# Performance work log

Measured on AMD Instinct MI355X. Metric: run time of the kernel, lower is better.

The kernel has to match this reference:

```python
import jax, jax.numpy as jnp
import numpy as np

H = 2048
NBINS = 256

def setup_inputs() -> dict:
    key = jax.random.key(0)
    k1, k2, k3, k4 = jax.random.split(key, 4)
    input_data = jax.random.uniform(k1, (1, 3, H, H), jnp.float32, -1.0, 1.0)
    target_data = jax.random.uniform(k2, (1, 3, H, H), jnp.float32, -1.0, 1.0)
    mask_src = (jax.random.uniform(k3, (1, 1, H, H)) > 0.5).astype(jnp.float32)
    mask_tar = (jax.random.uniform(k4, (1, 1, H, H)) > 0.5).astype(jnp.float32)
    return {"input_data": input_data, "target_data": target_data,
            "mask_src": mask_src, "mask_tar": mask_tar}


def _de_norm(x):
    # (x+1)/2 clamped to [0,1]
    return jnp.clip((x + 1.0) * 0.5, 0.0, 1.0)


def _masked_cdf(img, mask):
    # img: [3,H,W] in [0,255]; mask: [H,W] 0/1 weights.
    # Equivalent to np.histogram(masked_pixels, bins=256, range=(0,255)) per
    # channel followed by normalized cumsum: weighted bincount over all pixels.
    bins = jnp.clip(jnp.floor(img * (NBINS / 255.0)).astype(jnp.int32), 0, NBINS - 1)
    offs = bins + (jnp.arange(3, dtype=jnp.int32) * NBINS)[:, None, None]
    w = jnp.broadcast_to(mask, img.shape).reshape(-1)
    hist = jax.ops.segment_sum(w, offs.reshape(-1), num_segments=3 * NBINS)
    hist = hist.reshape(3, NBINS)
    cdf = jnp.cumsum(hist, axis=1)
    total = jnp.maximum(cdf[:, -1:], 1.0)  # number of masked pixels
    return cdf / total


def _cal_trans(dst_cdf, ref_cdf):
    # Faithful vectorization of PSGAN cal_trans: for i in 1..255, table[i] is
    # the first j in 1..255 with ref_cdf[j-1] <= dst_cdf[i] <= ref_cdf[j],
    # else i; table[0]=0, table[255]=255.
    j0 = jnp.searchsorted(ref_cdf, dst_cdf, side='left')
    cand = jnp.clip(j0, 1, NBINS - 1)
    ok = (ref_cdf[cand - 1] <= dst_cdf) & (ref_cdf[cand] >= dst_cdf)
    idx = jnp.arange(NBINS)
    table = jnp.where(ok, cand, idx)
    table = table.at[0].set(0).at[NBINS - 1].set(NBINS - 1)
    return table


def _histogram_loss(input_data, target_data, mask_src, mask_tar):
    inp = _de_norm(input_data)[0] * 255.0   # [3,H,W]
    tar = _de_norm(target_data)[0] * 255.0  # [3,H,W]
    ms = mask_src[0, 0]  # [H,W]
    mt = mask_tar[0, 0]
    input_masked = inp * ms
    target_masked = tar * mt

    cdf_dst = _masked_cdf(input_masked, ms)   # [3,256]
    cdf_ref = _masked_cdf(target_masked, mt)  # [3,256]
    tables = jax.vmap(_cal_trans)(cdf_dst, cdf_ref)  # [3,256] int

    # remap masked pixels through per-channel LUT (int() truncation)
    pix = jnp.clip(input_masked.astype(jnp.int32), 0, NBINS - 1)  # [3,H,W]
    matched = jnp.take_along_axis(tables, pix.reshape(3, -1), axis=1)
    matched = matched.reshape(input_masked.shape).astype(input_masked.dtype)
    input_match = jnp.where(ms[None] != 0, matched, input_masked)
    input_match = jax.lax.stop_gradient(input_match)  # to_var(requires_grad=False)

    return jnp.mean(jnp.abs(input_masked - input_match))


def reference(input_data, target_data, mask_src, mask_tar):
    return _histogram_loss(input_data, target_data, mask_src, mask_tar)
```

## Files before the change

### kernel.cpp

```cpp
#include <hip/hip_runtime.h>

#define HH 2048
#define NPIX (HH * HH)
#define NBINS 256
#define NRBINS 512
#define NQ (NPIX / 4)

#define BLOCKS 512
#define THREADS 512
#define ITERS (NQ / (BLOCKS * THREADS))

#define CNT_SHIFT 42
#define FRAC_MASK ((1ULL << CNT_SHIFT) - 1)

#define GPK_WORDS (3 * NRBINS)
#define GHT_WORDS (3 * NBINS)
#define WS_ZERO_BYTES (GPK_WORDS * 8 + GHT_WORDS * 4)

__device__ __forceinline__ float denorm255(float x) {
    return fminf(fmaxf((x + 1.0f) * 0.5f, 0.0f), 1.0f) * 255.0f;
}

__global__ __launch_bounds__(THREADS, 2) void fused_hist(
        const float* __restrict__ in, const float* __restrict__ tar,
        const float* __restrict__ ms, const float* __restrict__ mt,
        unsigned long long* __restrict__ gpk, unsigned* __restrict__ ght) {
    __shared__ unsigned long long lpk[3 * NRBINS];
    __shared__ unsigned lht[3 * NBINS];
    for (int i = threadIdx.x; i < 3 * NRBINS; i += THREADS) lpk[i] = 0ULL;
    for (int i = threadIdx.x; i < 3 * NBINS; i += THREADS) lht[i] = 0u;
    __syncthreads();

    const float BSCALE = 256.0f / 255.0f;
    const float FSCALE = 4194304.0f;
    const int stride = BLOCKS * THREADS;
    int idx = blockIdx.x * THREADS + threadIdx.x;

    float4 cm  = ((const float4*)ms)[idx];
    float4 ct  = ((const float4*)mt)[idx];
    float4 ca0 = ((const float4*)(in))[idx];
    float4 ca1 = ((const float4*)(in + NPIX))[idx];
    float4 ca2 = ((const float4*)(in + 2 * NPIX))[idx];
    float4 cb0 = ((const float4*)(tar))[idx];
    float4 cb1 = ((const float4*)(tar + NPIX))[idx];
    float4 cb2 = ((const float4*)(tar + 2 * NPIX))[idx];

    #pragma unroll
    for (int s = 0; s < ITERS; ++s) {
        float4 nm, nt4, na0, na1, na2, nb0, nb1, nb2;
        const int nidx = idx + stride;
        if (s < ITERS - 1) {
            nm  = ((const float4*)ms)[nidx];
            nt4 = ((const float4*)mt)[nidx];
            na0 = ((const float4*)(in))[nidx];
            na1 = ((const float4*)(in + NPIX))[nidx];
            na2 = ((const float4*)(in + 2 * NPIX))[nidx];
            nb0 = ((const float4*)(tar))[nidx];
            nb1 = ((const float4*)(tar + NPIX))[nidx];
            nb2 = ((const float4*)(tar + 2 * NPIX))[nidx];
        }

        const float mv[4] = {cm.x, cm.y, cm.z, cm.w};
        const float tv[4] = {ct.x, ct.y, ct.z, ct.w};
        const float av[3][4] = {{ca0.x, ca0.y, ca0.z, ca0.w},
                                {ca1.x, ca1.y, ca1.z, ca1.w},
                                {ca2.x, ca2.y, ca2.z, ca2.w}};
        const float bv[3][4] = {{cb0.x, cb0.y, cb0.z, cb0.w},
                                {cb1.x, cb1.y, cb1.z, cb1.w},
                                {cb2.x, cb2.y, cb2.z, cb2.w}};

        #pragma unroll
        for (int ch = 0; ch < 3; ++ch) {
            #pragma unroll
            for (int k = 0; k < 4; ++k) {
                float v = denorm255(av[ch][k]);
                int hb = min((int)(v * BSCALE), NBINS - 1);
                int tb = (int)v;
                unsigned fr = (unsigned)((v - (float)tb) * FSCALE);
                unsigned long long pk =
                    (1ULL << CNT_SHIFT) | (unsigned long long)fr;
                pk = (mv[k] != 0.0f) ? pk : 0ULL;
                atomicAdd(&lpk[ch * NRBINS + hb + tb], pk);

                float w = denorm255(bv[ch][k]);
                int wb = min((int)(w * BSCALE), NBINS - 1);
                atomicAdd(&lht[ch * NBINS + wb], (tv[k] != 0.0f) ? 1u : 0u);
            }
        }
        if (s < ITERS - 1) {
            cm = nm; ct = nt4;
            ca0 = na0; ca1 = na1; ca2 = na2;
            cb0 = nb0; cb1 = nb1; cb2 = nb2;
        }
        idx = nidx;
    }
    __syncthreads();
    for (int i = threadIdx.x; i < 3 * NRBINS; i += THREADS) {
        unsigned long long p = lpk[i];
        if (p) atomicAdd(&gpk[i], p);
    }
    for (int i = threadIdx.x; i < 3 * NBINS; i += THREADS) {
        unsigned h = lht[i];
        if (h) atomicAdd(&ght[i], h);
    }
}

__global__ __launch_bounds__(NBINS) void table_loss(
        const unsigned long long* __restrict__ gpk,
        const unsigned* __restrict__ ght, float* __restrict__ out) {
    __shared__ float cdf[6][NBINS];
    __shared__ float tot[6];
    const int t = threadIdx.x;

    unsigned long long pe[3], po[3];
    #pragma unroll
    for (int ch = 0; ch < 3; ++ch) {
        pe[ch] = gpk[ch * NRBINS + 2 * t];
        po[ch] = gpk[ch * NRBINS + 2 * t + 1];
        unsigned long long pp = (t > 0) ? gpk[ch * NRBINS + 2 * t - 1] : 0ULL;
        cdf[ch][t] = (float)((pe[ch] >> CNT_SHIFT) + (pp >> CNT_SHIFT));
        cdf[3 + ch][t] = (float)ght[ch * NBINS + t];
    }
    __syncthreads();
    #pragma unroll
    for (int off = 1; off < NBINS; off <<= 1) {
        float add[6];
        #pragma unroll
        for (int j = 0; j < 6; ++j) add[j] = (t >= off) ? cdf[j][t - off] : 0.0f;
        __syncthreads();
        #pragma unroll
        for (int j = 0; j < 6; ++j) cdf[j][t] += add[j];
        __syncthreads();
    }
    if (t < 6) tot[t] = fmaxf(cdf[t][NBINS - 1], 1.0f);
    __syncthreads();
    #pragma unroll
    for (int j = 0; j < 6; ++j) cdf[j][t] = cdf[j][t] / tot[j];
    __syncthreads();

    double lsum = 0.0;
    #pragma unroll
    for (int ch = 0; ch < 3; ++ch) {
        const float d = cdf[ch][t];
        const float* ref = cdf[3 + ch];
        int lo = 0, hi = NBINS;
        while (lo < hi) {
            int mid = (lo + hi) >> 1;
            if (ref[mid] < d) lo = mid + 1; else hi = mid;
        }
        int cand = min(max(lo, 1), NBINS - 1);
        int T = (ref[cand - 1] <= d && ref[cand] >= d) ? cand : t;
        if (t == 0) T = 0;
        if (t == NBINS - 1) T = NBINS - 1;

        const int b = t;
        const double c =
            (double)((pe[ch] >> CNT_SHIFT) + (po[ch] >> CNT_SHIFT));
        const double F =
            (double)((pe[ch] & FRAC_MASK) + (po[ch] & FRAC_MASK)) *
            (1.0 / 4194304.0);
        lsum += (T <= b) ? (c * (double)(b - T) + F)
                         : (c * (double)(T - b) - F);
    }
    #pragma unroll
    for (int off = 32; off; off >>= 1) lsum += __shfl_down(lsum, off, 64);
    __shared__ double wsum[4];
    if ((t & 63) == 0) wsum[t >> 6] = lsum;
    __syncthreads();
    if (t == 0)
        out[0] = (float)((wsum[0] + wsum[1] + wsum[2] + wsum[3]) /
                         (double)(3 * NPIX));
}

extern "C" void kernel_launch(void* const* d_in, const int* in_sizes, int n_in,
                              void* d_out, int out_size, void* d_ws, size_t ws_size,
                              hipStream_t stream) {
    const float* in  = (const float*)d_in[0];
    const float* tar = (const float*)d_in[1];
    const float* ms  = (const float*)d_in[2];
    const float* mt  = (const float*)d_in[3];
    float* out = (float*)d_out;

    unsigned long long* gpk = (unsigned long long*)d_ws;
    unsigned* ght = (unsigned*)((char*)d_ws + GPK_WORDS * 8);

    hipMemsetAsync(d_ws, 0, WS_ZERO_BYTES, stream);
    fused_hist<<<BLOCKS, THREADS, 0, stream>>>(in, tar, ms, mt, gpk, ght);
    table_loss<<<1, NBINS, 0, stream>>>(gpk, ght, out);
}
```

Baseline: 160.7 us.

## Split source and target histograms into separate block roles with mask-predicated atomics

The fused histogram kernel now launches twice as many blocks, half building the source packed histogram and half the target histogram, each reading only its own four input planes. Explicit register prefetching is removed in favour of more resident blocks (launch bounds raised to 8 per CU) and less shared memory per block. Atomics are skipped for unmasked pixels instead of adding zero, which roughly halves the number of LDS atomics on this input. The cost is more global merge atomics from twice the blocks and divergent branches inside wavefronts.

```diff
diff --git a/kernel.cpp b/kernel.cpp
--- a/kernel.cpp
+++ b/kernel.cpp
@@ -6,9 +6,14 @@
 #define NRBINS 512
 #define NQ (NPIX / 4)
 
-#define BLOCKS 512
 #define THREADS 512
-#define ITERS (NQ / (BLOCKS * THREADS))
+#define SRC_BLOCKS 1024
+#define TAR_BLOCKS 1024
+#define GRID (SRC_BLOCKS + TAR_BLOCKS)
+#define SRC_CHUNK (NQ / SRC_BLOCKS)
+#define TAR_CHUNK (NQ / TAR_BLOCKS)
+#define SRC_ITERS (SRC_CHUNK / THREADS)
+#define TAR_ITERS (TAR_CHUNK / THREADS)
 
 #define CNT_SHIFT 42
 #define FRAC_MASK ((1ULL << CNT_SHIFT) - 1)
@@ -21,87 +26,82 @@
     return fminf(fmaxf((x + 1.0f) * 0.5f, 0.0f), 1.0f) * 255.0f;
 }
 
-__global__ __launch_bounds__(THREADS, 2) void fused_hist(
-        const float* __restrict__ in, const float* __restrict__ tar,
+__global__ __launch_bounds__(THREADS, 8) void fused_hist(
+        const float* __restrict__ in, const float* __restrict__ tarp,
         const float* __restrict__ ms, const float* __restrict__ mt,
         unsigned long long* __restrict__ gpk, unsigned* __restrict__ ght) {
     __shared__ unsigned long long lpk[3 * NRBINS];
-    __shared__ unsigned lht[3 * NBINS];
-    for (int i = threadIdx.x; i < 3 * NRBINS; i += THREADS) lpk[i] = 0ULL;
-    for (int i = threadIdx.x; i < 3 * NBINS; i += THREADS) lht[i] = 0u;
-    __syncthreads();
-
     const float BSCALE = 256.0f / 255.0f;
     const float FSCALE = 4194304.0f;
-    const int stride = BLOCKS * THREADS;
-    int idx = blockIdx.x * THREADS + threadIdx.x;
 
-    float4 cm  = ((const float4*)ms)[idx];
-    float4 ct  = ((const float4*)mt)[idx];
-    float4 ca0 = ((const float4*)(in))[idx];
-    float4 ca1 = ((const float4*)(in + NPIX))[idx];
-    float4 ca2 = ((const float4*)(in + 2 * NPIX))[idx];
-    float4 cb0 = ((const float4*)(tar))[idx];
-    float4 cb1 = ((const float4*)(tar + NPIX))[idx];
-    float4 cb2 = ((const float4*)(tar + 2 * NPIX))[idx];
-
-    #pragma unroll
-    for (int s = 0; s < ITERS; ++s) {
-        float4 nm, nt4, na0, na1, na2, nb0, nb1, nb2;
-        const int nidx = idx + stride;
-        if (s < ITERS - 1) {
-            nm  = ((const float4*)ms)[nidx];
-            nt4 = ((const float4*)mt)[nidx];
-            na0 = ((const float4*)(in))[nidx];
-            na1 = ((const float4*)(in + NPIX))[nidx];
-            na2 = ((const float4*)(in + 2 * NPIX))[nidx];
-            nb0 = ((const float4*)(tar))[nidx];
-            nb1 = ((const float4*)(tar + NPIX))[nidx];
-            nb2 = ((const float4*)(tar + 2 * NPIX))[nidx];
-        }
-
-        const float mv[4] = {cm.x, cm.y, cm.z, cm.w};
-        const float tv[4] = {ct.x, ct.y, ct.z, ct.w};
-        const float av[3][4] = {{ca0.x, ca0.y, ca0.z, ca0.w},
-                                {ca1.x, ca1.y, ca1.z, ca1.w},
-                                {ca2.x, ca2.y, ca2.z, ca2.w}};
-        const float bv[3][4] = {{cb0.x, cb0.y, cb0.z, cb0.w},
-                                {cb1.x, cb1.y, cb1.z, cb1.w},
-                                {cb2.x, cb2.y, cb2.z, cb2.w}};
-
+    if (blockIdx.x < SRC_BLOCKS) {
+        for (int i = threadIdx.x; i < 3 * NRBINS; i += THREADS) lpk[i] = 0ULL;
+        __syncthreads();
+        const int base = blockIdx.x * SRC_CHUNK + threadIdx.x;
         #pragma unroll
-        for (int ch = 0; ch < 3; ++ch) {
+        for (int s = 0; s < SRC_ITERS; ++s) {
+            const int idx = base + s * THREADS;
+            float4 m4 = ((const float4*)ms)[idx];
+            float4 a0 = ((const float4*)(in))[idx];
+            float4 a1 = ((const float4*)(in + NPIX))[idx];
+            float4 a2 = ((const float4*)(in + 2 * NPIX))[idx];
+            const float mv[4] = {m4.x, m4.y, m4.z, m4.w};
+            const float av[3][4] = {{a0.x, a0.y, a0.z, a0.w},
+                                    {a1.x, a1.y, a1.z, a1.w},
+                                    {a2.x, a2.y, a2.z, a2.w}};
             #pragma unroll
-            for (int k = 0; k < 4; ++k) {
-                float v = denorm255(av[ch][k]);
-                int hb = min((int)(v * BSCALE), NBINS - 1);
-                int tb = (int)v;
-                unsigned fr = (unsigned)((v - (float)tb) * FSCALE);
-                unsigned long long pk =
-                    (1ULL << CNT_SHIFT) | (unsigned long long)fr;
-                pk = (mv[k] != 0.0f) ? pk : 0ULL;
-                atomicAdd(&lpk[ch * NRBINS + hb + tb], pk);
-
-                float w = denorm255(bv[ch][k]);
-                int wb = min((int)(w * BSCALE), NBINS - 1);
-                atomicAdd(&lht[ch * NBINS + wb], (tv[k] != 0.0f) ? 1u : 0u);
+            for (int ch = 0; ch < 3; ++ch) {
+                #pragma unroll
+                for (int k = 0; k < 4; ++k) {
+                    if (mv[k] != 0.0f) {
+                        float v = denorm255(av[ch][k]);
+                        int hb = min((int)(v * BSCALE), NBINS - 1);
+                        int tb = (int)v;
+                        unsigned fr = (unsigned)((v - (float)tb) * FSCALE);
+                        atomicAdd(&lpk[ch * NRBINS + hb + tb],
+                                  (1ULL << CNT_SHIFT) | (unsigned long long)fr);
+                    }
+                }
             }
         }
-        if (s < ITERS - 1) {
-            cm = nm; ct = nt4;
-            ca0 = na0; ca1 = na1; ca2 = na2;
-            cb0 = nb0; cb1 = nb1; cb2 = nb2;
+        __syncthreads();
+        for (int i = threadIdx.x; i < 3 * NRBINS; i += THREADS) {
+            unsigned long long p = lpk[i];
+            if (p) atomicAdd(&gpk[i], p);
         }
-        idx = nidx;
-    }
-    __syncthreads();
-    for (int i = threadIdx.x; i < 3 * NRBINS; i += THREADS) {
-        unsigned long long p = lpk[i];
-        if (p) atomicAdd(&gpk[i], p);
-    }
-    for (int i = threadIdx.x; i < 3 * NBINS; i += THREADS) {
-        unsigned h = lht[i];
-        if (h) atomicAdd(&ght[i], h);
+    } else {
+        unsigned* lht = (unsigned*)lpk;
+        for (int i = threadIdx.x; i < 3 * NBINS; i += THREADS) lht[i] = 0u;
+        __syncthreads();
+        const int base = (blockIdx.x - SRC_BLOCKS) * TAR_CHUNK + threadIdx.x;
+        #pragma unroll
+        for (int s = 0; s < TAR_ITERS; ++s) {
+            const int idx = base + s * THREADS;
+            float4 t4 = ((const float4*)mt)[idx];
+            float4 b0 = ((const float4*)(tarp))[idx];
+            float4 b1 = ((const float4*)(tarp + NPIX))[idx];
+            float4 b2 = ((const float4*)(tarp + 2 * NPIX))[idx];
+            const float tv[4] = {t4.x, t4.y, t4.z, t4.w};
+            const float bv[3][4] = {{b0.x, b0.y, b0.z, b0.w},
+                                    {b1.x, b1.y, b1.z, b1.w},
+                                    {b2.x, b2.y, b2.z, b2.w}};
+            #pragma unroll
+            for (int ch = 0; ch < 3; ++ch) {
+                #pragma unroll
+                for (int k = 0; k < 4; ++k) {
+                    if (tv[k] != 0.0f) {
+                        float w = denorm255(bv[ch][k]);
+                        int wb = min((int)(w * BSCALE), NBINS - 1);
+                        atomicAdd(&lht[ch * NBINS + wb], 1u);
+                    }
+                }
+            }
+        }
+        __syncthreads();
+        for (int i = threadIdx.x; i < 3 * NBINS; i += THREADS) {
+            unsigned h = lht[i];
+            if (h) atomicAdd(&ght[i], h);
+        }
     }
 }
 
@@ -185,6 +185,6 @@
     unsigned* ght = (unsigned*)((char*)d_ws + GPK_WORDS * 8);
 
     hipMemsetAsync(d_ws, 0, WS_ZERO_BYTES, stream);
-    fused_hist<<<BLOCKS, THREADS, 0, stream>>>(in, tar, ms, mt, gpk, ght);
+    fused_hist<<<GRID, THREADS, 0, stream>>>(in, tar, ms, mt, gpk, ght);
     table_loss<<<1, NBINS, 0, stream>>>(gpk, ght, out);
 }
```

New measurement: 171.0 us. 1.06x slower.

## Split global histogram atomics into partial copies and skip masked-out atomics

Applied to the files above, without the earlier changes.

Per-block shared histograms are flushed into one of 32 partial global copies instead of a single histogram, which spreads out global atomic contention. A new reduce kernel sums the partials before the table/loss kernel runs. The shared-memory atomics are now predicated on the mask, so masked-out pixels issue no atomic at all. Launch bounds also allow more resident blocks. The cost is an extra kernel launch and a larger memset of the partial buffers.

```diff
diff --git a/kernel.cpp b/kernel.cpp
--- a/kernel.cpp
+++ b/kernel.cpp
@@ -13,18 +13,19 @@
 #define CNT_SHIFT 42
 #define FRAC_MASK ((1ULL << CNT_SHIFT) - 1)
 
-#define GPK_WORDS (3 * NRBINS)
-#define GHT_WORDS (3 * NBINS)
-#define WS_ZERO_BYTES (GPK_WORDS * 8 + GHT_WORDS * 4)
+#define NWORDS (3 * NRBINS + 3 * NBINS)
+#define NSPLIT 32
+#define PART_BYTES ((size_t)NSPLIT * NWORDS * 8)
+#define WS_ZERO_BYTES (PART_BYTES + (size_t)NWORDS * 8)
 
 __device__ __forceinline__ float denorm255(float x) {
     return fminf(fmaxf((x + 1.0f) * 0.5f, 0.0f), 1.0f) * 255.0f;
 }
 
-__global__ __launch_bounds__(THREADS, 2) void fused_hist(
-        const float* __restrict__ in, const float* __restrict__ tar,
+__global__ __launch_bounds__(THREADS, 8) void fused_hist(
+        const float* __restrict__ in, const float* __restrict__ tarp,
         const float* __restrict__ ms, const float* __restrict__ mt,
-        unsigned long long* __restrict__ gpk, unsigned* __restrict__ ght) {
+        unsigned long long* __restrict__ part) {
     __shared__ unsigned long long lpk[3 * NRBINS];
     __shared__ unsigned lht[3 * NBINS];
     for (int i = threadIdx.x; i < 3 * NRBINS; i += THREADS) lpk[i] = 0ULL;
@@ -41,9 +42,9 @@
     float4 ca0 = ((const float4*)(in))[idx];
     float4 ca1 = ((const float4*)(in + NPIX))[idx];
     float4 ca2 = ((const float4*)(in + 2 * NPIX))[idx];
-    float4 cb0 = ((const float4*)(tar))[idx];
-    float4 cb1 = ((const float4*)(tar + NPIX))[idx];
-    float4 cb2 = ((const float4*)(tar + 2 * NPIX))[idx];
+    float4 cb0 = ((const float4*)(tarp))[idx];
+    float4 cb1 = ((const float4*)(tarp + NPIX))[idx];
+    float4 cb2 = ((const float4*)(tarp + 2 * NPIX))[idx];
 
     #pragma unroll
     for (int s = 0; s < ITERS; ++s) {
@@ -55,9 +56,9 @@
             na0 = ((const float4*)(in))[nidx];
             na1 = ((const float4*)(in + NPIX))[nidx];
             na2 = ((const float4*)(in + 2 * NPIX))[nidx];
-            nb0 = ((const float4*)(tar))[nidx];
-            nb1 = ((const float4*)(tar + NPIX))[nidx];
-            nb2 = ((const float4*)(tar + 2 * NPIX))[nidx];
+            nb0 = ((const float4*)(tarp))[nidx];
+            nb1 = ((const float4*)(tarp + NPIX))[nidx];
+            nb2 = ((const float4*)(tarp + 2 * NPIX))[nidx];
         }
 
         const float mv[4] = {cm.x, cm.y, cm.z, cm.w};
@@ -73,18 +74,19 @@
         for (int ch = 0; ch < 3; ++ch) {
             #pragma unroll
             for (int k = 0; k < 4; ++k) {
-                float v = denorm255(av[ch][k]);
-                int hb = min((int)(v * BSCALE), NBINS - 1);
-                int tb = (int)v;
-                unsigned fr = (unsigned)((v - (float)tb) * FSCALE);
-                unsigned long long pk =
-                    (1ULL << CNT_SHIFT) | (unsigned long long)fr;
-                pk = (mv[k] != 0.0f) ? pk : 0ULL;
-                atomicAdd(&lpk[ch * NRBINS + hb + tb], pk);
-
-                float w = denorm255(bv[ch][k]);
-                int wb = min((int)(w * BSCALE), NBINS - 1);
-                atomicAdd(&lht[ch * NBINS + wb], (tv[k] != 0.0f) ? 1u : 0u);
+                if (mv[k] != 0.0f) {
+                    float v = denorm255(av[ch][k]);
+                    int hb = min((int)(v * BSCALE), NBINS - 1);
+                    int tb = (int)v;
+                    unsigned fr = (unsigned)((v - (float)tb) * FSCALE);
+                    atomicAdd(&lpk[ch * NRBINS + hb + tb],
+                              (1ULL << CNT_SHIFT) | (unsigned long long)fr);
+                }
+                if (tv[k] != 0.0f) {
+                    float w = denorm255(bv[ch][k]);
+                    int wb = min((int)(w * BSCALE), NBINS - 1);
+                    atomicAdd(&lht[ch * NBINS + wb], 1u);
+                }
             }
         }
         if (s < ITERS - 1) {
@@ -95,19 +97,30 @@
         idx = nidx;
     }
     __syncthreads();
+
+    unsigned long long* my = part + (size_t)(blockIdx.x % NSPLIT) * NWORDS;
     for (int i = threadIdx.x; i < 3 * NRBINS; i += THREADS) {
         unsigned long long p = lpk[i];
-        if (p) atomicAdd(&gpk[i], p);
+        if (p) atomicAdd(&my[i], p);
     }
     for (int i = threadIdx.x; i < 3 * NBINS; i += THREADS) {
         unsigned h = lht[i];
-        if (h) atomicAdd(&ght[i], h);
-    }
+        if (h) atomicAdd(&my[3 * NRBINS + i], (unsigned long long)h);
+    }
+}
+
+__global__ __launch_bounds__(256) void reduce_kernel(
+        const unsigned long long* __restrict__ part,
+        unsigned long long* __restrict__ gfin) {
+    const int w = blockIdx.x * 256 + threadIdx.x;
+    unsigned long long s = 0ULL;
+    #pragma unroll
+    for (int c = 0; c < NSPLIT; ++c) s += part[(size_t)c * NWORDS + w];
+    gfin[w] = s;
 }
 
 __global__ __launch_bounds__(NBINS) void table_loss(
-        const unsigned long long* __restrict__ gpk,
-        const unsigned* __restrict__ ght, float* __restrict__ out) {
+        const unsigned long long* __restrict__ gfin, float* __restrict__ out) {
     __shared__ float cdf[6][NBINS];
     __shared__ float tot[6];
     const int t = threadIdx.x;
@@ -115,11 +128,11 @@
     unsigned long long pe[3], po[3];
     #pragma unroll
     for (int ch = 0; ch < 3; ++ch) {
-        pe[ch] = gpk[ch * NRBINS + 2 * t];
-        po[ch] = gpk[ch * NRBINS + 2 * t + 1];
-        unsigned long long pp = (t > 0) ? gpk[ch * NRBINS + 2 * t - 1] : 0ULL;
+        pe[ch] = gfin[ch * NRBINS + 2 * t];
+        po[ch] = gfin[ch * NRBINS + 2 * t + 1];
+        unsigned long long pp = (t > 0) ? gfin[ch * NRBINS + 2 * t - 1] : 0ULL;
         cdf[ch][t] = (float)((pe[ch] >> CNT_SHIFT) + (pp >> CNT_SHIFT));
-        cdf[3 + ch][t] = (float)ght[ch * NBINS + t];
+        cdf[3 + ch][t] = (float)gfin[3 * NRBINS + ch * NBINS + t];
     }
     __syncthreads();
     #pragma unroll
@@ -181,10 +194,11 @@
     const float* mt  = (const float*)d_in[3];
     float* out = (float*)d_out;
 
-    unsigned long long* gpk = (unsigned long long*)d_ws;
-    unsigned* ght = (unsigned*)((char*)d_ws + GPK_WORDS * 8);
+    unsigned long long* part = (unsigned long long*)d_ws;
+    unsigned long long* gfin = (unsigned long long*)((char*)d_ws + PART_BYTES);
 
     hipMemsetAsync(d_ws, 0, WS_ZERO_BYTES, stream);
-    fused_hist<<<BLOCKS, THREADS, 0, stream>>>(in, tar, ms, mt, gpk, ght);
-    table_loss<<<1, NBINS, 0, stream>>>(gpk, ght, out);
-}
+    fused_hist<<<BLOCKS, THREADS, 0, stream>>>(in, tar, ms, mt, part);
+    reduce_kernel<<<NWORDS / 256, 256, 0, stream>>>(part, gfin);
+    table_loss<<<1, NBINS, 0, stream>>>(gfin, out);
+}
```

After: 185.3 us. +15.3%, slower.
